# Kernel optimization log

Hardware: AMD Instinct MI355X
Metric: run time of the kernel (lower is better)

Reference implementation:

```python
import jax, jax.numpy as jnp
import numpy as np

B, C, H, W = 8, 256, 64, 64
D = C // 8  # 32


def setup_inputs() -> dict:
    key = jax.random.key(0)
    ks = jax.random.split(key, 6)
    s = 0.06  # ~1/sqrt(C): keeps q@k logits in a sane range so softmax is not one-hot
    x = jax.random.normal(ks[0], (B, C, H, W), dtype=jnp.float32)
    wq = jax.random.normal(ks[1], (D, C), dtype=jnp.float32) * s
    wk = jax.random.normal(ks[2], (D, C), dtype=jnp.float32) * s
    wv = jax.random.normal(ks[3], (D, C), dtype=jnp.float32) * s
    wo = jax.random.normal(ks[4], (C, D), dtype=jnp.float32) * s
    gamma = jax.random.uniform(ks[5], (1,), dtype=jnp.float32)
    return {"x": x, "wq": wq, "wk": wk, "wv": wv, "wo": wo, "gamma": gamma}


def reference(x, wq, wk, wv, wo, gamma):
    b, c, h, w = x.shape
    n = h * w
    xf = x.reshape(b, c, n)                          # [B,C,N]
    # 1x1 convs == channel matmuls
    q = jnp.einsum('dc,bcn->bnd', wq, xf)            # [B,N,D]
    k = jnp.einsum('dc,bcn->bdn', wk, xf)            # [B,D,N]
    v = jnp.einsum('dc,bcn->bdn', wv, xf)            # [B,D,N]
    # full NxN attention, softmax over keys (last axis), no 1/sqrt(d) scaling (as in source)
    attn = jax.nn.softmax(jnp.einsum('bnd,bdm->bnm', q, k), axis=-1)  # [B,N,N]
    out = jnp.einsum('bdm,bnm->bdn', v, attn)        # v @ attn^T -> [B,D,N]
    o = jnp.einsum('cd,bdn->bcn', wo, out).reshape(b, c, h, w)
    return o * gamma + x
```

## Files before the change

### kernel.cpp

```cpp
#include <hip/hip_runtime.h>
#include <hip/hip_bf16.h>
#include <hip/hip_fp16.h>


typedef _Float16 f16;
typedef f16 f16x8 __attribute__((ext_vector_type(8)));
typedef __fp16 h16x2 __attribute__((ext_vector_type(2)));
typedef float f32x4 __attribute__((ext_vector_type(4)));

#define B_ 8
#define C_ 256
#define N_ 4096
#define D_ 32

__global__ __launch_bounds__(256) void qkv_kernel(
    const float* __restrict__ x, const float* __restrict__ wq,
    const float* __restrict__ wk, const float* __restrict__ wv,
    f16* __restrict__ Q, f16* __restrict__ K, f16* __restrict__ Vt)
{
    __shared__ float wls[256][36];
    const int tid = threadIdx.x;
    const int ntile = blockIdx.x, mat = blockIdx.y, b = blockIdx.z;
    const float* w = (mat == 0) ? wq : (mat == 1 ? wk : wv);

    #pragma unroll
    for (int k = 0; k < 32; ++k) wls[tid][k] = w[k * 256 + tid];
    __syncthreads();

    const int n  = ntile * 64 + (tid & 63);
    const int d0 = (tid >> 6) * 8;
    const float* xb = x + (size_t)b * C_ * N_ + n;

    float acc[8];
    #pragma unroll
    for (int j = 0; j < 8; ++j) acc[j] = 0.f;

    float xn = xb[0];
    for (int c = 0; c < 256; ++c) {
        const float xv = xn;
        if (c < 255) xn = xb[(size_t)(c + 1) * N_];
        const float4 wa = *(const float4*)&wls[c][d0];
        const float4 wb = *(const float4*)&wls[c][d0 + 4];
        acc[0] += wa.x * xv; acc[1] += wa.y * xv; acc[2] += wa.z * xv; acc[3] += wa.w * xv;
        acc[4] += wb.x * xv; acc[5] += wb.y * xv; acc[6] += wb.z * xv; acc[7] += wb.w * xv;
    }

    if (mat < 2) {
        f16* op = (mat == 0 ? Q : K) + ((size_t)b * N_ + n) * D_ + d0;
        f16x8 h;
        #pragma unroll
        for (int j = 0; j < 8; ++j) h[j] = (f16)acc[j];
        *(f16x8*)op = h;
    } else {
        const int p = n & 31;
        const int cidx = (n & ~31) + 8 * ((p >> 2) & 3) + 4 * ((p >> 4) & 1) + (p & 3);
        f16* vb = Vt + ((size_t)b * D_ + d0) * N_ + cidx;
        #pragma unroll
        for (int j = 0; j < 8; ++j) vb[(size_t)j * N_] = (f16)acc[j];
    }
}

__global__ __launch_bounds__(256, 4) void flash_kernel(
    const f16* __restrict__ Qh, const f16* __restrict__ Kh,
    const f16* __restrict__ Vth, float* __restrict__ Opart,
    float* __restrict__ Ml, int kcnt, int kch)
{
    const int lane = threadIdx.x & 63;
    const int wid = threadIdx.x >> 6;
    const int b = blockIdx.x, kc = blockIdx.y, qt = blockIdx.z;
    const int q0 = qt * 128 + wid * 32;
    const int l15 = lane & 15, g = lane >> 4;

    const f16* qp = Qh + ((size_t)b * N_ + q0 + l15) * D_ + g * 8;
    const f16x8 qf0 = *(const f16x8*)qp;
    const f16x8 qf1 = *(const f16x8*)(qp + (size_t)16 * D_);

    const f16* kp = Kh + ((size_t)b * N_ + (size_t)kc * kch + l15) * D_ + g * 8;
    const f16* vp = Vth + ((size_t)b * D_ + l15) * N_ + (size_t)kc * kch + g * 8;

    f32x4 O00 = {0.f, 0.f, 0.f, 0.f};
    f32x4 O01 = O00, O10 = O00, O11 = O00;
    float m0 = -3e38f, m1 = -3e38f, l0 = 0.f, l1 = 0.f;
    const int NW = kch >> 5;

    f16x8 kf0 = *(const f16x8*)kp;
    f16x8 kf1 = *(const f16x8*)(kp + (size_t)16 * D_);
    f16x8 vf0 = *(const f16x8*)vp;
    f16x8 vf1 = *(const f16x8*)(vp + (size_t)16 * N_);

    for (int w = 0; w < NW; ++w) {
        const int wn = (w + 1 < NW) ? (w + 1) : w;
        const f16* kpn = kp + (size_t)wn * 32 * D_;
        const f16* vpn = vp + (size_t)wn * 32;
        const f16x8 kn0 = *(const f16x8*)kpn;
        const f16x8 kn1 = *(const f16x8*)(kpn + (size_t)16 * D_);
        const f16x8 vn0 = *(const f16x8*)vpn;
        const f16x8 vn1 = *(const f16x8*)(vpn + (size_t)16 * N_);

        const f32x4 z = {0.f, 0.f, 0.f, 0.f};
        f32x4 s00 = __builtin_amdgcn_mfma_f32_16x16x32_f16(kf0, qf0, z, 0, 0, 0);
        f32x4 s01 = __builtin_amdgcn_mfma_f32_16x16x32_f16(kf1, qf0, z, 0, 0, 0);
        f32x4 s10 = __builtin_amdgcn_mfma_f32_16x16x32_f16(kf0, qf1, z, 0, 0, 0);
        f32x4 s11 = __builtin_amdgcn_mfma_f32_16x16x32_f16(kf1, qf1, z, 0, 0, 0);

        union { f16x8 v; h16x2 h[4]; } pb0, pb1;
        {
            float mx = fmaxf(fmaxf(fmaxf(s00[0], s00[1]), fmaxf(s00[2], s00[3])),
                             fmaxf(fmaxf(s01[0], s01[1]), fmaxf(s01[2], s01[3])));
            mx = fmaxf(mx, __shfl_xor(mx, 16));
            mx = fmaxf(mx, __shfl_xor(mx, 32));
            if (__any(mx > m0 + 7.f)) {
                const float nm = fmaxf(m0, mx);
                const float f = __expf(m0 - nm);
                m0 = nm; l0 *= f;
                #pragma unroll
                for (int r = 0; r < 4; ++r) { O00[r] *= f; O01[r] *= f; }
            }
            const float p0 = __expf(s00[0] - m0), p1 = __expf(s00[1] - m0);
            const float p2 = __expf(s00[2] - m0), p3 = __expf(s00[3] - m0);
            const float p4 = __expf(s01[0] - m0), p5 = __expf(s01[1] - m0);
            const float p6 = __expf(s01[2] - m0), p7 = __expf(s01[3] - m0);
            l0 += ((p0 + p1) + (p2 + p3)) + ((p4 + p5) + (p6 + p7));
            pb0.h[0] = __builtin_amdgcn_cvt_pkrtz(p0, p1);
            pb0.h[1] = __builtin_amdgcn_cvt_pkrtz(p2, p3);
            pb0.h[2] = __builtin_amdgcn_cvt_pkrtz(p4, p5);
            pb0.h[3] = __builtin_amdgcn_cvt_pkrtz(p6, p7);
        }
        {
            float mx = fmaxf(fmaxf(fmaxf(s10[0], s10[1]), fmaxf(s10[2], s10[3])),
                             fmaxf(fmaxf(s11[0], s11[1]), fmaxf(s11[2], s11[3])));
            mx = fmaxf(mx, __shfl_xor(mx, 16));
            mx = fmaxf(mx, __shfl_xor(mx, 32));
            if (__any(mx > m1 + 7.f)) {
                const float nm = fmaxf(m1, mx);
                const float f = __expf(m1 - nm);
                m1 = nm; l1 *= f;
                #pragma unroll
                for (int r = 0; r < 4; ++r) { O10[r] *= f; O11[r] *= f; }
            }
            const float p0 = __expf(s10[0] - m1), p1 = __expf(s10[1] - m1);
            const float p2 = __expf(s10[2] - m1), p3 = __expf(s10[3] - m1);
            const float p4 = __expf(s11[0] - m1), p5 = __expf(s11[1] - m1);
            const float p6 = __expf(s11[2] - m1), p7 = __expf(s11[3] - m1);
            l1 += ((p0 + p1) + (p2 + p3)) + ((p4 + p5) + (p6 + p7));
            pb1.h[0] = __builtin_amdgcn_cvt_pkrtz(p0, p1);
            pb1.h[1] = __builtin_amdgcn_cvt_pkrtz(p2, p3);
            pb1.h[2] = __builtin_amdgcn_cvt_pkrtz(p4, p5);
            pb1.h[3] = __builtin_amdgcn_cvt_pkrtz(p6, p7);
        }

        O00 = __builtin_amdgcn_mfma_f32_16x16x32_f16(vf0, pb0.v, O00, 0, 0, 0);
        O01 = __builtin_amdgcn_mfma_f32_16x16x32_f16(vf1, pb0.v, O01, 0, 0, 0);
        O10 = __builtin_amdgcn_mfma_f32_16x16x32_f16(vf0, pb1.v, O10, 0, 0, 0);
        O11 = __builtin_amdgcn_mfma_f32_16x16x32_f16(vf1, pb1.v, O11, 0, 0, 0);

        kf0 = kn0; kf1 = kn1; vf0 = vn0; vf1 = vn1;
    }

    l0 += __shfl_xor(l0, 16); l0 += __shfl_xor(l0, 32);
    l1 += __shfl_xor(l1, 16); l1 += __shfl_xor(l1, 32);

    float* ob = Opart + (size_t)(b * kcnt + kc) * D_ * N_ + q0 + l15;
    #pragma unroll
    for (int r = 0; r < 4; ++r) {
        ob[(size_t)(g * 4 + r) * N_]           = O00[r];
        ob[(size_t)(16 + g * 4 + r) * N_]      = O01[r];
        ob[(size_t)(g * 4 + r) * N_ + 16]      = O10[r];
        ob[(size_t)(16 + g * 4 + r) * N_ + 16] = O11[r];
    }
    if (lane < 16) {
        float2* mp = (float2*)(Ml + ((size_t)(b * kcnt + kc) * N_ + q0 + l15) * 2);
        mp[0]  = make_float2(m0, l0);
        mp[16] = make_float2(m1, l1);
    }
}

__global__ __launch_bounds__(256) void merge_proj_kernel(
    const float* __restrict__ Opart, const float* __restrict__ Ml,
    const float* __restrict__ wo, const float* __restrict__ gamma,
    const float* __restrict__ x, float* __restrict__ out, int kcnt)
{
    __shared__ float oc[64][33];
    __shared__ float wot[32][260];
    const int tid = threadIdx.x;
    const int n0 = blockIdx.x * 64, b = blockIdx.y;

    for (int i = tid; i < 256 * 32; i += 256) {
        const int c = i >> 5, d = i & 31;
        wot[d][c] = wo[i];
    }

    const int nl = tid & 63;
    const int n = n0 + nl;
    const int grp = tid >> 6;

    {
        const int d0 = grp * 8;
        float mstar = -3e38f;
        for (int c8 = 0; c8 < kcnt; ++c8) {
            const float2 ml = *(const float2*)(Ml + (((size_t)b * kcnt + c8) * N_ + n) * 2);
            mstar = fmaxf(mstar, ml.x);
        }
        float acc[8];
        #pragma unroll
        for (int j = 0; j < 8; ++j) acc[j] = 0.f;
        float lstar = 0.f;
        for (int c8 = 0; c8 < kcnt; ++c8) {
            const float2 ml = *(const float2*)(Ml + (((size_t)b * kcnt + c8) * N_ + n) * 2);
            const float wgt = __expf(ml.x - mstar);
            lstar += wgt * ml.y;
            const float* op = Opart + (((size_t)b * kcnt + c8) * D_ + d0) * N_ + n;
            #pragma unroll
            for (int j = 0; j < 8; ++j) acc[j] += wgt * op[(size_t)j * N_];
        }
        const float inv = 1.0f / lstar;
        #pragma unroll
        for (int j = 0; j < 8; ++j) oc[nl][d0 + j] = acc[j] * inv;
    }
    __syncthreads();

    const float gmv = gamma[0];
    const float* xb = x + (size_t)b * C_ * N_ + n;
    float* ob = out + (size_t)b * C_ * N_ + n;
    for (int cg = 0; cg < 8; ++cg) {
        const int c0 = grp * 64 + cg * 8;
        float acc8[8];
        #pragma unroll
        for (int j = 0; j < 8; ++j) acc8[j] = 0.f;
        for (int d = 0; d < 32; ++d) {
            const float ov = oc[nl][d];
            const float4 w0 = *(const float4*)&wot[d][c0];
            const float4 w1 = *(const float4*)&wot[d][c0 + 4];
            acc8[0] += w0.x * ov; acc8[1] += w0.y * ov; acc8[2] += w0.z * ov; acc8[3] += w0.w * ov;
            acc8[4] += w1.x * ov; acc8[5] += w1.y * ov; acc8[6] += w1.z * ov; acc8[7] += w1.w * ov;
        }
        #pragma unroll
        for (int j = 0; j < 8; ++j) {
            const size_t off = (size_t)(c0 + j) * N_;
            ob[off] = gmv * acc8[j] + xb[off];
        }
    }
}

extern "C" void kernel_launch(void* const* d_in, const int* in_sizes, int n_in,
                              void* d_out, int out_size, void* d_ws, size_t ws_size,
                              hipStream_t stream) {
    const float* x  = (const float*)d_in[0];
    const float* wq = (const float*)d_in[1];
    const float* wk = (const float*)d_in[2];
    const float* wv = (const float*)d_in[3];
    const float* wo = (const float*)d_in[4];
    const float* gm = (const float*)d_in[5];
    float* out = (float*)d_out;

    int kcnt = 4;
    while (kcnt > 1) {
        const size_t need = 3 * (size_t)B_ * N_ * D_ * 2
                          + (size_t)B_ * kcnt * N_ * D_ * 4
                          + (size_t)B_ * kcnt * N_ * 2 * 4;
        if (need <= ws_size) break;
        kcnt >>= 1;
    }
    const int kch = N_ / kcnt;

    f16* Qb  = (f16*)d_ws;
    f16* Kb  = Qb + (size_t)B_ * N_ * D_;
    f16* Vtb = Kb + (size_t)B_ * N_ * D_;
    float* Opart = (float*)(Vtb + (size_t)B_ * N_ * D_);
    float* Mlb   = Opart + (size_t)B_ * kcnt * N_ * D_;

    qkv_kernel<<<dim3(64, 3, B_), 256, 0, stream>>>(x, wq, wk, wv, Qb, Kb, Vtb);
    flash_kernel<<<dim3(B_, kcnt, N_ / 128), 256, 0, stream>>>(Qb, Kb, Vtb, Opart, Mlb,
                                                               kcnt, kch);
    merge_proj_kernel<<<dim3(64, B_), 256, 0, stream>>>(Opart, Mlb, wo, gm, x, out, kcnt);
}
```

Measured before the change: 186.9 us.

## Use MFMA for QKV and output projections, exp2 softmax, more key splits

Adds a prep kernel that converts the weights to fp16 and folds log2e into Wq and gamma into Wo. The QKV projection and the merge/output projection now run on MFMA instead of scalar FMAs. The flash loop uses raw v_exp_f32 (exp2), raises the lazy-rescale threshold, adds s_setprio around the MFMAs, raises occupancy to 8 blocks per CU, and doubles the key splits to 8. This trades fp32 precision in the projections for fewer ALU cycles, at the cost of more partial-output traffic in the merge.

```diff
diff --git a/kernel.cpp b/kernel.cpp
--- a/kernel.cpp
+++ b/kernel.cpp
@@ -5,6 +5,7 @@
 
 typedef _Float16 f16;
 typedef f16 f16x8 __attribute__((ext_vector_type(8)));
+typedef f16 f16x4 __attribute__((ext_vector_type(4)));
 typedef __fp16 h16x2 __attribute__((ext_vector_type(2)));
 typedef float f32x4 __attribute__((ext_vector_type(4)));
 
@@ -12,55 +13,97 @@
 #define C_ 256
 #define N_ 4096
 #define D_ 32
-
-__global__ __launch_bounds__(256) void qkv_kernel(
-    const float* __restrict__ x, const float* __restrict__ wq,
-    const float* __restrict__ wk, const float* __restrict__ wv,
+#define LOG2E 1.44269504088896f
+
+__device__ __forceinline__ float fexp2(float x) {
+    float r;
+    asm volatile("v_exp_f32 %0, %1" : "=v"(r) : "v"(x));
+    return r;
+}
+
+__global__ __launch_bounds__(256) void prep_kernel(
+    const float* __restrict__ wq, const float* __restrict__ wk,
+    const float* __restrict__ wv, const float* __restrict__ wo,
+    const float* __restrict__ gamma,
+    f16* __restrict__ whq, f16* __restrict__ whk,
+    f16* __restrict__ whv, f16* __restrict__ woh)
+{
+    const int i = blockIdx.x * 256 + threadIdx.x;
+    whq[i] = (f16)(wq[i] * LOG2E);
+    whk[i] = (f16)wk[i];
+    whv[i] = (f16)wv[i];
+    woh[i] = (f16)(wo[i] * gamma[0]);
+}
+
+__global__ __launch_bounds__(256) void qkv2_kernel(
+    const float* __restrict__ x, const f16* __restrict__ whq,
+    const f16* __restrict__ whk, const f16* __restrict__ whv,
     f16* __restrict__ Q, f16* __restrict__ K, f16* __restrict__ Vt)
 {
-    __shared__ float wls[256][36];
-    const int tid = threadIdx.x;
-    const int ntile = blockIdx.x, mat = blockIdx.y, b = blockIdx.z;
-    const float* w = (mat == 0) ? wq : (mat == 1 ? wk : wv);
-
-    #pragma unroll
-    for (int k = 0; k < 32; ++k) wls[tid][k] = w[k * 256 + tid];
-    __syncthreads();
-
-    const int n  = ntile * 64 + (tid & 63);
-    const int d0 = (tid >> 6) * 8;
+    const int lane = threadIdx.x & 63, wid = threadIdx.x >> 6;
+    const int b = blockIdx.y;
+    const int n0 = blockIdx.x * 64 + wid * 16;
+    const int l15 = lane & 15, g = lane >> 4;
+    const int n = n0 + l15;
+
     const float* xb = x + (size_t)b * C_ * N_ + n;
-
-    float acc[8];
-    #pragma unroll
-    for (int j = 0; j < 8; ++j) acc[j] = 0.f;
-
-    float xn = xb[0];
-    for (int c = 0; c < 256; ++c) {
-        const float xv = xn;
-        if (c < 255) xn = xb[(size_t)(c + 1) * N_];
-        const float4 wa = *(const float4*)&wls[c][d0];
-        const float4 wb = *(const float4*)&wls[c][d0 + 4];
-        acc[0] += wa.x * xv; acc[1] += wa.y * xv; acc[2] += wa.z * xv; acc[3] += wa.w * xv;
-        acc[4] += wb.x * xv; acc[5] += wb.y * xv; acc[6] += wb.z * xv; acc[7] += wb.w * xv;
-    }
-
-    if (mat < 2) {
-        f16* op = (mat == 0 ? Q : K) + ((size_t)b * N_ + n) * D_ + d0;
-        f16x8 h;
-        #pragma unroll
-        for (int j = 0; j < 8; ++j) h[j] = (f16)acc[j];
-        *(f16x8*)op = h;
-    } else {
+    f32x4 aq0 = {0.f, 0.f, 0.f, 0.f};
+    f32x4 aq1 = aq0, ak0 = aq0, ak1 = aq0, av0 = aq0, av1 = aq0;
+
+    #pragma unroll
+    for (int ks = 0; ks < 8; ++ks) {
+        const int c0 = ks * 32 + g * 8;
+        float xr[8];
+        #pragma unroll
+        for (int j = 0; j < 8; ++j) xr[j] = xb[(size_t)(c0 + j) * N_];
+        union { f16x8 v; h16x2 h[4]; } xf;
+        #pragma unroll
+        for (int j = 0; j < 4; ++j)
+            xf.h[j] = __builtin_amdgcn_cvt_pkrtz(xr[2 * j], xr[2 * j + 1]);
+
+        const int woff = l15 * 256 + c0;
+        const f16x8 fq0 = *(const f16x8*)(whq + woff);
+        const f16x8 fq1 = *(const f16x8*)(whq + woff + 16 * 256);
+        const f16x8 fk0 = *(const f16x8*)(whk + woff);
+        const f16x8 fk1 = *(const f16x8*)(whk + woff + 16 * 256);
+        const f16x8 fv0 = *(const f16x8*)(whv + woff);
+        const f16x8 fv1 = *(const f16x8*)(whv + woff + 16 * 256);
+
+        aq0 = __builtin_amdgcn_mfma_f32_16x16x32_f16(fq0, xf.v, aq0, 0, 0, 0);
+        aq1 = __builtin_amdgcn_mfma_f32_16x16x32_f16(fq1, xf.v, aq1, 0, 0, 0);
+        ak0 = __builtin_amdgcn_mfma_f32_16x16x32_f16(fk0, xf.v, ak0, 0, 0, 0);
+        ak1 = __builtin_amdgcn_mfma_f32_16x16x32_f16(fk1, xf.v, ak1, 0, 0, 0);
+        av0 = __builtin_amdgcn_mfma_f32_16x16x32_f16(fv0, xf.v, av0, 0, 0, 0);
+        av1 = __builtin_amdgcn_mfma_f32_16x16x32_f16(fv1, xf.v, av1, 0, 0, 0);
+    }
+
+    {
+        f16x4 h0, h1;
+        #pragma unroll
+        for (int r = 0; r < 4; ++r) { h0[r] = (f16)aq0[r]; h1[r] = (f16)aq1[r]; }
+        f16* qp = Q + ((size_t)b * N_ + n) * D_ + 4 * g;
+        *(f16x4*)qp = h0; *(f16x4*)(qp + 16) = h1;
+    }
+    {
+        f16x4 h0, h1;
+        #pragma unroll
+        for (int r = 0; r < 4; ++r) { h0[r] = (f16)ak0[r]; h1[r] = (f16)ak1[r]; }
+        f16* kp = K + ((size_t)b * N_ + n) * D_ + 4 * g;
+        *(f16x4*)kp = h0; *(f16x4*)(kp + 16) = h1;
+    }
+    {
         const int p = n & 31;
         const int cidx = (n & ~31) + 8 * ((p >> 2) & 3) + 4 * ((p >> 4) & 1) + (p & 3);
-        f16* vb = Vt + ((size_t)b * D_ + d0) * N_ + cidx;
-        #pragma unroll
-        for (int j = 0; j < 8; ++j) vb[(size_t)j * N_] = (f16)acc[j];
-    }
-}
-
-__global__ __launch_bounds__(256, 4) void flash_kernel(
+        f16* vb = Vt + ((size_t)b * D_ + 4 * g) * N_ + cidx;
+        #pragma unroll
+        for (int r = 0; r < 4; ++r) {
+            vb[(size_t)r * N_]        = (f16)av0[r];
+            vb[(size_t)(16 + r) * N_] = (f16)av1[r];
+        }
+    }
+}
+
+__global__ __launch_bounds__(256, 8) void flash_kernel(
     const f16* __restrict__ Qh, const f16* __restrict__ Kh,
     const f16* __restrict__ Vth, float* __restrict__ Opart,
     float* __restrict__ Ml, int kcnt, int kch)
@@ -98,10 +141,12 @@
         const f16x8 vn1 = *(const f16x8*)(vpn + (size_t)16 * N_);
 
         const f32x4 z = {0.f, 0.f, 0.f, 0.f};
+        __builtin_amdgcn_s_setprio(1);
         f32x4 s00 = __builtin_amdgcn_mfma_f32_16x16x32_f16(kf0, qf0, z, 0, 0, 0);
         f32x4 s01 = __builtin_amdgcn_mfma_f32_16x16x32_f16(kf1, qf0, z, 0, 0, 0);
         f32x4 s10 = __builtin_amdgcn_mfma_f32_16x16x32_f16(kf0, qf1, z, 0, 0, 0);
         f32x4 s11 = __builtin_amdgcn_mfma_f32_16x16x32_f16(kf1, qf1, z, 0, 0, 0);
+        __builtin_amdgcn_s_setprio(0);
 
         union { f16x8 v; h16x2 h[4]; } pb0, pb1;
         {
@@ -109,17 +154,17 @@
                              fmaxf(fmaxf(s01[0], s01[1]), fmaxf(s01[2], s01[3])));
             mx = fmaxf(mx, __shfl_xor(mx, 16));
             mx = fmaxf(mx, __shfl_xor(mx, 32));
-            if (__any(mx > m0 + 7.f)) {
+            if (__any(mx > m0 + 10.f)) {
                 const float nm = fmaxf(m0, mx);
-                const float f = __expf(m0 - nm);
+                const float f = fexp2(m0 - nm);
                 m0 = nm; l0 *= f;
                 #pragma unroll
                 for (int r = 0; r < 4; ++r) { O00[r] *= f; O01[r] *= f; }
             }
-            const float p0 = __expf(s00[0] - m0), p1 = __expf(s00[1] - m0);
-            const float p2 = __expf(s00[2] - m0), p3 = __expf(s00[3] - m0);
-            const float p4 = __expf(s01[0] - m0), p5 = __expf(s01[1] - m0);
-            const float p6 = __expf(s01[2] - m0), p7 = __expf(s01[3] - m0);
+            const float p0 = fexp2(s00[0] - m0), p1 = fexp2(s00[1] - m0);
+            const float p2 = fexp2(s00[2] - m0), p3 = fexp2(s00[3] - m0);
+            const float p4 = fexp2(s01[0] - m0), p5 = fexp2(s01[1] - m0);
+            const float p6 = fexp2(s01[2] - m0), p7 = fexp2(s01[3] - m0);
             l0 += ((p0 + p1) + (p2 + p3)) + ((p4 + p5) + (p6 + p7));
             pb0.h[0] = __builtin_amdgcn_cvt_pkrtz(p0, p1);
             pb0.h[1] = __builtin_amdgcn_cvt_pkrtz(p2, p3);
@@ -131,17 +176,17 @@
                              fmaxf(fmaxf(s11[0], s11[1]), fmaxf(s11[2], s11[3])));
             mx = fmaxf(mx, __shfl_xor(mx, 16));
             mx = fmaxf(mx, __shfl_xor(mx, 32));
-            if (__any(mx > m1 + 7.f)) {
+            if (__any(mx > m1 + 10.f)) {
                 const float nm = fmaxf(m1, mx);
-                const float f = __expf(m1 - nm);
+                const float f = fexp2(m1 - nm);
                 m1 = nm; l1 *= f;
                 #pragma unroll
                 for (int r = 0; r < 4; ++r) { O10[r] *= f; O11[r] *= f; }
             }
-            const float p0 = __expf(s10[0] - m1), p1 = __expf(s10[1] - m1);
-            const float p2 = __expf(s10[2] - m1), p3 = __expf(s10[3] - m1);
-            const float p4 = __expf(s11[0] - m1), p5 = __expf(s11[1] - m1);
-            const float p6 = __expf(s11[2] - m1), p7 = __expf(s11[3] - m1);
+            const float p0 = fexp2(s10[0] - m1), p1 = fexp2(s10[1] - m1);
+            const float p2 = fexp2(s10[2] - m1), p3 = fexp2(s10[3] - m1);
+            const float p4 = fexp2(s11[0] - m1), p5 = fexp2(s11[1] - m1);
+            const float p6 = fexp2(s11[2] - m1), p7 = fexp2(s11[3] - m1);
             l1 += ((p0 + p1) + (p2 + p3)) + ((p4 + p5) + (p6 + p7));
             pb1.h[0] = __builtin_amdgcn_cvt_pkrtz(p0, p1);
             pb1.h[1] = __builtin_amdgcn_cvt_pkrtz(p2, p3);
@@ -149,10 +194,12 @@
             pb1.h[3] = __builtin_amdgcn_cvt_pkrtz(p6, p7);
         }
 
+        __builtin_amdgcn_s_setprio(1);
         O00 = __builtin_amdgcn_mfma_f32_16x16x32_f16(vf0, pb0.v, O00, 0, 0, 0);
         O01 = __builtin_amdgcn_mfma_f32_16x16x32_f16(vf1, pb0.v, O01, 0, 0, 0);
         O10 = __builtin_amdgcn_mfma_f32_16x16x32_f16(vf0, pb1.v, O10, 0, 0, 0);
         O11 = __builtin_amdgcn_mfma_f32_16x16x32_f16(vf1, pb1.v, O11, 0, 0, 0);
+        __builtin_amdgcn_s_setprio(0);
 
         kf0 = kn0; kf1 = kn1; vf0 = vn0; vf1 = vn1;
     }
@@ -175,69 +222,50 @@
     }
 }
 
-__global__ __launch_bounds__(256) void merge_proj_kernel(
+__global__ __launch_bounds__(256) void merge2_kernel(
     const float* __restrict__ Opart, const float* __restrict__ Ml,
-    const float* __restrict__ wo, const float* __restrict__ gamma,
-    const float* __restrict__ x, float* __restrict__ out, int kcnt)
+    const f16* __restrict__ woh, const float* __restrict__ x,
+    float* __restrict__ out, int kcnt)
 {
-    __shared__ float oc[64][33];
-    __shared__ float wot[32][260];
-    const int tid = threadIdx.x;
-    const int n0 = blockIdx.x * 64, b = blockIdx.y;
-
-    for (int i = tid; i < 256 * 32; i += 256) {
-        const int c = i >> 5, d = i & 31;
-        wot[d][c] = wo[i];
-    }
-
-    const int nl = tid & 63;
-    const int n = n0 + nl;
-    const int grp = tid >> 6;
-
-    {
-        const int d0 = grp * 8;
-        float mstar = -3e38f;
-        for (int c8 = 0; c8 < kcnt; ++c8) {
-            const float2 ml = *(const float2*)(Ml + (((size_t)b * kcnt + c8) * N_ + n) * 2);
-            mstar = fmaxf(mstar, ml.x);
-        }
-        float acc[8];
-        #pragma unroll
-        for (int j = 0; j < 8; ++j) acc[j] = 0.f;
-        float lstar = 0.f;
-        for (int c8 = 0; c8 < kcnt; ++c8) {
-            const float2 ml = *(const float2*)(Ml + (((size_t)b * kcnt + c8) * N_ + n) * 2);
-            const float wgt = __expf(ml.x - mstar);
-            lstar += wgt * ml.y;
-            const float* op = Opart + (((size_t)b * kcnt + c8) * D_ + d0) * N_ + n;
-            #pragma unroll
-            for (int j = 0; j < 8; ++j) acc[j] += wgt * op[(size_t)j * N_];
-        }
-        const float inv = 1.0f / lstar;
-        #pragma unroll
-        for (int j = 0; j < 8; ++j) oc[nl][d0 + j] = acc[j] * inv;
-    }
-    __syncthreads();
-
-    const float gmv = gamma[0];
-    const float* xb = x + (size_t)b * C_ * N_ + n;
-    float* ob = out + (size_t)b * C_ * N_ + n;
-    for (int cg = 0; cg < 8; ++cg) {
-        const int c0 = grp * 64 + cg * 8;
-        float acc8[8];
-        #pragma unroll
-        for (int j = 0; j < 8; ++j) acc8[j] = 0.f;
-        for (int d = 0; d < 32; ++d) {
-            const float ov = oc[nl][d];
-            const float4 w0 = *(const float4*)&wot[d][c0];
-            const float4 w1 = *(const float4*)&wot[d][c0 + 4];
-            acc8[0] += w0.x * ov; acc8[1] += w0.y * ov; acc8[2] += w0.z * ov; acc8[3] += w0.w * ov;
-            acc8[4] += w1.x * ov; acc8[5] += w1.y * ov; acc8[6] += w1.z * ov; acc8[7] += w1.w * ov;
-        }
-        #pragma unroll
-        for (int j = 0; j < 8; ++j) {
-            const size_t off = (size_t)(c0 + j) * N_;
-            ob[off] = gmv * acc8[j] + xb[off];
+    const int lane = threadIdx.x & 63, wid = threadIdx.x >> 6;
+    const int b = blockIdx.y;
+    const int n0 = blockIdx.x * 64 + wid * 16;
+    const int l15 = lane & 15, g = lane >> 4;
+    const int n = n0 + l15;
+
+    float mstar = -3e38f;
+    for (int kc = 0; kc < kcnt; ++kc)
+        mstar = fmaxf(mstar, Ml[(((size_t)b * kcnt + kc) * N_ + n) * 2]);
+
+    float acc[8];
+    #pragma unroll
+    for (int j = 0; j < 8; ++j) acc[j] = 0.f;
+    float lstar = 0.f;
+    for (int kc = 0; kc < kcnt; ++kc) {
+        const float2 ml = *(const float2*)(Ml + (((size_t)b * kcnt + kc) * N_ + n) * 2);
+        const float wgt = fexp2(ml.x - mstar);
+        lstar += wgt * ml.y;
+        const float* op = Opart + (((size_t)b * kcnt + kc) * D_ + g * 8) * N_ + n;
+        #pragma unroll
+        for (int j = 0; j < 8; ++j) acc[j] += wgt * op[(size_t)j * N_];
+    }
+    const float inv = 1.0f / lstar;
+    union { f16x8 v; h16x2 h[4]; } oc;
+    #pragma unroll
+    for (int j = 0; j < 4; ++j)
+        oc.h[j] = __builtin_amdgcn_cvt_pkrtz(acc[2 * j] * inv, acc[2 * j + 1] * inv);
+
+    const float* xb = x + (size_t)b * C_ * N_;
+    float* ob = out + (size_t)b * C_ * N_;
+    const f32x4 z = {0.f, 0.f, 0.f, 0.f};
+    #pragma unroll
+    for (int ct = 0; ct < 16; ++ct) {
+        const f16x8 wf = *(const f16x8*)(woh + (ct * 16 + l15) * 32 + g * 8);
+        const f32x4 o = __builtin_amdgcn_mfma_f32_16x16x32_f16(wf, oc.v, z, 0, 0, 0);
+        #pragma unroll
+        for (int r = 0; r < 4; ++r) {
+            const size_t off = (size_t)(ct * 16 + 4 * g + r) * N_ + n;
+            ob[off] = o[r] + xb[off];
         }
     }
 }
@@ -253,24 +281,30 @@
     const float* gm = (const float*)d_in[5];
     float* out = (float*)d_out;
 
-    int kcnt = 4;
+    int kcnt = 8;
     while (kcnt > 1) {
-        const size_t need = 3 * (size_t)B_ * N_ * D_ * 2
-                          + (size_t)B_ * kcnt * N_ * D_ * 4
-                          + (size_t)B_ * kcnt * N_ * 2 * 4;
+        const size_t need = 65536
+                          + 3 * (size_t)B_ * N_ * D_ * 2
+                          + (size_t)kcnt * B_ * N_ * D_ * 4
+                          + (size_t)kcnt * B_ * N_ * 2 * 4;
         if (need <= ws_size) break;
         kcnt >>= 1;
     }
     const int kch = N_ / kcnt;
 
-    f16* Qb  = (f16*)d_ws;
+    f16* whq = (f16*)d_ws;
+    f16* whk = whq + 8192;
+    f16* whv = whk + 8192;
+    f16* woh = whv + 8192;
+    f16* Qb  = woh + 8192;
     f16* Kb  = Qb + (size_t)B_ * N_ * D_;
     f16* Vtb = Kb + (size_t)B_ * N_ * D_;
     float* Opart = (float*)(Vtb + (size_t)B_ * N_ * D_);
-    float* Mlb   = Opart + (size_t)B_ * kcnt * N_ * D_;
-
-    qkv_kernel<<<dim3(64, 3, B_), 256, 0, stream>>>(x, wq, wk, wv, Qb, Kb, Vtb);
+    float* Mlb   = Opart + (size_t)kcnt * B_ * N_ * D_;
+
+    prep_kernel<<<32, 256, 0, stream>>>(wq, wk, wv, wo, gm, whq, whk, whv, woh);
+    qkv2_kernel<<<dim3(64, B_), 256, 0, stream>>>(x, whq, whk, whv, Qb, Kb, Vtb);
     flash_kernel<<<dim3(B_, kcnt, N_ / 128), 256, 0, stream>>>(Qb, Kb, Vtb, Opart, Mlb,
                                                                kcnt, kch);
-    merge_proj_kernel<<<dim3(64, B_), 256, 0, stream>>>(Opart, Mlb, wo, gm, x, out, kcnt);
-}
+    merge2_kernel<<<dim3(64, B_), 256, 0, stream>>>(Opart, Mlb, woh, x, out, kcnt);
+}
```

Result: slower. 237.8 us (+27.2%).
